# Optimization experiments

Hardware: AMD Instinct MI355X
Metric: run time of the kernel (lower is better)

## Reference

```python
import jax, jax.numpy as jnp
import numpy as np


def setup_inputs() -> dict:
    key = jax.random.key(0)
    k1, k2 = jax.random.split(key)
    B, C, P, D, K = 8, 8, 512, 256, 8192
    z = jax.random.normal(k1, (B, C, P, D), dtype=jnp.float32)
    # codebook initialized with std = 1/sqrt(dim), matching nn.init.normal_
    codebook = jax.random.normal(k2, (K, D), dtype=jnp.float32) / np.sqrt(D).astype(np.float32)
    return {"z": z, "codebook": codebook}


def reference(z, codebook):
    B, C, P, D = z.shape
    z_flat = z.reshape(-1, D)  # [N, D]
    # squared-L2 distances: ||z||^2 - 2 z.cb^T + ||cb||^2  -> [N, K]
    dist = (
        jnp.sum(z_flat * z_flat, axis=1, keepdims=True)
        - 2.0 * jnp.matmul(z_flat, codebook.T)
        + jnp.sum(codebook * codebook, axis=1)[None, :]
    )
    codes = jnp.argmin(dist, axis=1)  # [N]
    z_q = codebook[codes].reshape(B, C, P, D)
    commit_loss = 0.25 * jnp.mean((jax.lax.stop_gradient(z_q) - z) ** 2)
    codebook_loss = jnp.mean((z_q - jax.lax.stop_gradient(z)) ** 2)
    total_loss = commit_loss + 0.25 * codebook_loss
    # straight-through estimator
    z_q_st = z + jax.lax.stop_gradient(z_q - z)
    return (z_q_st, total_loss, codes)
```

## Files before the change

### kernel.cpp

```cpp
#include <hip/hip_runtime.h>
#include <hip/hip_fp16.h>
#include <float.h>

typedef _Float16 half8 __attribute__((ext_vector_type(8)));
typedef _Float16 half4 __attribute__((ext_vector_type(4)));
typedef float floatx4 __attribute__((ext_vector_type(4)));

#define DD 256
#define D4 64
#define KK 8192
#define NROWS 32768
#define BM 64
#define BM2 32
#define BM4 128
#define NELEM 8388608
#define TAU1 1.25e-2f
#define TAU2 2e-3f
#define NSLICE 8
#define SLICE_K 1024
#define NVS 16
#define VS_K 512
#define NBLOCKS1 1024
#define TILES_PER_BLOCK 4

#define WS_V9_BYTES      29360128
#define WS_CASCADE_BYTES 12582912
#define WS_SLICED2_BYTES 7800832
#define WS_R4_REFINE_BYTES 458768
#define WS_R4_FULL_BYTES   8849408

__global__ __launch_bounds__(256) void norms_kernel(
    const float* __restrict__ z, const float* __restrict__ cb,
    float* __restrict__ znorm, float* __restrict__ cbnorm)
{
    int wave = threadIdx.x >> 6;
    int lane = threadIdx.x & 63;
    int row = blockIdx.x * 4 + wave;
    const float4* src;
    float* dst;
    int r;
    if (row < NROWS) { src = (const float4*)z;  dst = znorm;  r = row; }
    else             { src = (const float4*)cb; dst = cbnorm; r = row - NROWS; }
    float4 v = src[(size_t)r * D4 + lane];
    float s = v.x*v.x + v.y*v.y + v.z*v.z + v.w*v.w;
    #pragma unroll
    for (int off = 1; off < 64; off <<= 1) s += __shfl_xor(s, off);
    if (lane == 0) dst[r] = s;
}

__global__ __launch_bounds__(256) void cbnorm_kernel(
    const float* __restrict__ cb, float* __restrict__ cbnorm)
{
    int wave = threadIdx.x >> 6;
    int lane = threadIdx.x & 63;
    int r = blockIdx.x * 4 + wave;
    float4 v = ((const float4*)cb)[(size_t)r * D4 + lane];
    float s = v.x*v.x + v.y*v.y + v.z*v.z + v.w*v.w;
    #pragma unroll
    for (int off = 1; off < 64; off <<= 1) s += __shfl_xor(s, off);
    if (lane == 0) cbnorm[r] = s;
}

__global__ __launch_bounds__(256) void preconv_kernel(
    const float* __restrict__ cb, _Float16* __restrict__ bhi, _Float16* __restrict__ blo)
{
    size_t e4 = (size_t)blockIdx.x * 256 + threadIdx.x;
    float4 v = ((const float4*)cb)[e4];
    float t0 = v.x * 16.f, t1 = v.y * 16.f, t2 = v.z * 16.f, t3 = v.w * 16.f;
    _Float16 h0 = (_Float16)t0, h1 = (_Float16)t1, h2 = (_Float16)t2, h3 = (_Float16)t3;
    _Float16 l0 = (_Float16)((t0 - (float)h0) * 2048.f);
    _Float16 l1 = (_Float16)((t1 - (float)h1) * 2048.f);
    _Float16 l2 = (_Float16)((t2 - (float)h2) * 2048.f);
    _Float16 l3 = (_Float16)((t3 - (float)h3) * 2048.f);
    reinterpret_cast<half4*>(bhi)[e4] = half4{h0, h1, h2, h3};
    reinterpret_cast<half4*>(blo)[e4] = half4{l0, l1, l2, l3};
}

__global__ __launch_bounds__(256) void preconv_z_kernel(
    const float* __restrict__ z, _Float16* __restrict__ zg, float* __restrict__ znorm)
{
    int gid = blockIdx.x * 256 + threadIdx.x;
    int row = gid >> 5;
    int g   = gid & 31;
    int r   = row & 63;
    const float4* src = (const float4*)z + (size_t)row * D4 + g * 2;
    float4 a = src[0], b = src[1];
    half8 h = { (_Float16)a.x, (_Float16)a.y, (_Float16)a.z, (_Float16)a.w,
                (_Float16)b.x, (_Float16)b.y, (_Float16)b.z, (_Float16)b.w };
    int gp = g ^ (r & 7);
    *reinterpret_cast<half8*>((char*)zg + (size_t)(row >> 6) * 32768 + r * 512 + gp * 16) = h;
    float s = a.x*a.x + a.y*a.y + a.z*a.z + a.w*a.w
            + b.x*b.x + b.y*b.y + b.z*b.z + b.w*b.w;
    #pragma unroll
    for (int off = 1; off < 32; off <<= 1) s += __shfl_xor(s, off);
    if ((threadIdx.x & 31) == 0) znorm[row] = s;
}

__global__ __launch_bounds__(256, 4) void vq_fp16_v11(
    const _Float16* __restrict__ zg,
    const _Float16* __restrict__ bhip, const float* __restrict__ cbnorm,
    float* __restrict__ pd, float* __restrict__ ps, int* __restrict__ pk)
{
    __shared__ _Float16 zt[BM * DD];

    const int tid  = threadIdx.x;
    const int lane = tid & 63;
    const int cg   = tid >> 6;
    const int l15  = lane & 15;
    const int lhi  = lane >> 4;
    const int slice = blockIdx.x & 7;
    const int grp   = blockIdx.x >> 3;

    const int A0 = l15 * 512 + ((lhi ^ (l15 & 3)) << 4) + (((l15 >> 2) & 1) << 6);
    int Ar[4];
    #pragma unroll
    for (int rf = 0; rf < 4; ++rf) Ar[rf] = A0 + rf * 8192;
    const char* zbase = (const char*)zt;

    const half8* bp = (const half8*)bhip + ((size_t)(slice * SLICE_K + cg * 32 + l15) * 32 + lhi);
    const float* cnp = cbnorm + slice * SLICE_K + cg * 32 + l15;
    const int kbase = slice * SLICE_K + cg * 32 + l15;

    #pragma unroll 1
    for (int j = 0; j < TILES_PER_BLOCK; ++j) {
        const int tileIdx = grp * TILES_PER_BLOCK + j;
        const int rowBase = tileIdx * BM;

        __syncthreads();
        {
            const float4* src = (const float4*)((const char*)zg + (size_t)tileIdx * 32768);
            float4* dst = (float4*)zt;
            #pragma unroll
            for (int i = 0; i < 8; ++i) dst[i * 256 + tid] = src[i * 256 + tid];
        }

        float bestd[4][4], secd[4][4];
        int   bestk[4][4];
        #pragma unroll
        for (int rf = 0; rf < 4; ++rf)
            #pragma unroll
            for (int reg = 0; reg < 4; ++reg) {
                bestd[rf][reg] = FLT_MAX; secd[rf][reg] = FLT_MAX; bestk[rf][reg] = 0;
            }

        __syncthreads();

        #pragma unroll 1
        for (int kt = 0; kt < SLICE_K / 128; ++kt) {
            floatx4 acc[4][2];
            #pragma unroll
            for (int rf = 0; rf < 4; ++rf)
                #pragma unroll
                for (int cf = 0; cf < 2; ++cf)
                    acc[rf][cf] = floatx4{0.f, 0.f, 0.f, 0.f};

            const half8* b0 = bp + kt * 4096;
            const half8* b1 = b0 + 512;

            #pragma unroll 2
            for (int dc = 0; dc < 8; ++dc) {
                half8 f0 = b0[dc * 4];
                half8 f1 = b1[dc * 4];
                #pragma unroll
                for (int rf = 0; rf < 4; ++rf) {
                    half8 a = *reinterpret_cast<const half8*>(zbase + (Ar[rf] ^ (dc << 6)));
                    acc[rf][0] = __builtin_amdgcn_mfma_f32_16x16x32_f16(a, f0, acc[rf][0], 0, 0, 0);
                    acc[rf][1] = __builtin_amdgcn_mfma_f32_16x16x32_f16(a, f1, acc[rf][1], 0, 0, 0);
                }
            }

            const float cn0 = cnp[kt * 128];
            const float cn1 = cnp[kt * 128 + 16];
            const int k0 = kbase + kt * 128;
            #pragma unroll
            for (int cf = 0; cf < 2; ++cf) {
                const float cn = cf ? cn1 : cn0;
                const int k = k0 + cf * 16;
                #pragma unroll
                for (int rf = 0; rf < 4; ++rf)
                    #pragma unroll
                    for (int reg = 0; reg < 4; ++reg) {
                        float m = fmaf(-0.125f, acc[rf][cf][reg], cn);
                        float w = fmaxf(bestd[rf][reg], m);
                        secd[rf][reg] = fminf(secd[rf][reg], w);
                        if (m < bestd[rf][reg]) { bestd[rf][reg] = m; bestk[rf][reg] = k; }
                    }
            }
        }

        #pragma unroll
        for (int off = 1; off < 16; off <<= 1) {
            #pragma unroll
            for (int rf = 0; rf < 4; ++rf)
                #pragma unroll
                for (int reg = 0; reg < 4; ++reg) {
                    float od = __shfl_xor(bestd[rf][reg], off);
                    int   ok = __shfl_xor(bestk[rf][reg], off);
                    float os = __shfl_xor(secd[rf][reg], off);
                    float hi = fmaxf(bestd[rf][reg], od);
                    secd[rf][reg] = fminf(fminf(secd[rf][reg], os), hi);
                    if (od < bestd[rf][reg] || (od == bestd[rf][reg] && ok < bestk[rf][reg])) {
                        bestd[rf][reg] = od; bestk[rf][reg] = ok;
                    }
                }
        }

        __syncthreads();
        float* dsc = reinterpret_cast<float*>(zt);
        int*   ksc = reinterpret_cast<int*>(zt) + 256;
        float* ssc = reinterpret_cast<float*>(zt) + 512;
        if (l15 == 0) {
            #pragma unroll
            for (int rf = 0; rf < 4; ++rf)
                #pragma unroll
                for (int reg = 0; reg < 4; ++reg) {
                    int rrow = rf * 16 + lhi * 4 + reg;
                    dsc[cg * 64 + rrow] = bestd[rf][reg];
                    ksc[cg * 64 + rrow] = bestk[rf][reg];
                    ssc[cg * 64 + rrow] = secd[rf][reg];
                }
        }
        __syncthreads();
        if (tid < 64) {
            float bd = dsc[tid];
            int   bk = ksc[tid];
            float sd = ssc[tid];
            #pragma unroll
            for (int c = 1; c < 4; ++c) {
                float od = dsc[c * 64 + tid];
                int   ok = ksc[c * 64 + tid];
                float os = ssc[c * 64 + tid];
                float hi = fmaxf(bd, od);
                sd = fminf(fminf(sd, os), hi);
                if (od < bd || (od == bd && ok < bk)) { bd = od; bk = ok; }
            }
            int row = rowBase + tid;
            pd[row * NSLICE + slice] = bd;
            ps[row * NSLICE + slice] = sd;
            pk[row * NSLICE + slice] = bk;
        }
    }
}

__global__ __launch_bounds__(256, 4) void vq_fp16_kernel(
    const float* __restrict__ z,
    const _Float16* __restrict__ bhip, const float* __restrict__ cbnorm,
    float* __restrict__ pd, float* __restrict__ ps, int* __restrict__ pk)
{
    __shared__ _Float16 zhi[BM * DD];
    const int tid  = threadIdx.x;
    const int lane = tid & 63;
    const int cg   = tid >> 6;
    const int l15  = lane & 15;
    const int lhi  = lane >> 4;
    const int slice = blockIdx.x & 7;
    const int grp   = blockIdx.x >> 3;
    const int sliceBase = slice * SLICE_K;

    int rowA[4];
    #pragma unroll
    for (int rf = 0; rf < 4; ++rf) rowA[rf] = rf * 16 + l15;

    #pragma unroll 1
    for (int j = 0; j < TILES_PER_BLOCK; ++j) {
        const int rowBase = (grp * TILES_PER_BLOCK + j) * BM;
        __syncthreads();
        #pragma unroll
        for (int i = 0; i < 16; ++i) {
            int gid = i * 256 + tid;
            int r   = gid >> 6;
            int c4  = gid & 63;
            float4 v = ((const float4*)z)[(size_t)(rowBase + r) * D4 + c4];
            _Float16 h0 = (_Float16)v.x, h1 = (_Float16)v.y,
                     h2 = (_Float16)v.z, h3 = (_Float16)v.w;
            int g = c4 >> 1;
            int byteOff = r * 512 + ((g ^ (r & 7)) << 4) + ((c4 & 1) << 3);
            *reinterpret_cast<half4*>(reinterpret_cast<char*>(zhi) + byteOff) = half4{h0, h1, h2, h3};
        }
        float bestd[4][4], secd[4][4];
        int   bestk[4][4];
        #pragma unroll
        for (int rf = 0; rf < 4; ++rf)
            #pragma unroll
            for (int reg = 0; reg < 4; ++reg) {
                bestd[rf][reg] = FLT_MAX; secd[rf][reg] = FLT_MAX; bestk[rf][reg] = 0;
            }
        __syncthreads();
        #pragma unroll 1
        for (int kt = 0; kt < SLICE_K / 128; ++kt) {
            floatx4 acc[4][2];
            #pragma unroll
            for (int rf = 0; rf < 4; ++rf)
                #pragma unroll
                for (int cf = 0; cf < 2; ++cf)
                    acc[rf][cf] = floatx4{0.f, 0.f, 0.f, 0.f};
            const int codeBase = sliceBase + kt * 128 + cg * 32 + l15;
            #pragma unroll 2
            for (int dc = 0; dc < 8; ++dc) {
                half8 bhi_f[2];
                #pragma unroll
                for (int cf = 0; cf < 2; ++cf) {
                    size_t off = (size_t)(codeBase + 16 * cf) * DD + dc * 32 + lhi * 8;
                    bhi_f[cf] = *reinterpret_cast<const half8*>(bhip + off);
                }
                #pragma unroll
                for (int rf = 0; rf < 4; ++rf) {
                    int g = dc * 4 + lhi;
                    int off = rowA[rf] * 512 + ((g ^ (rowA[rf] & 7)) << 4);
                    half8 ahi = *reinterpret_cast<const half8*>(reinterpret_cast<const char*>(zhi) + off);
                    #pragma unroll
                    for (int cf = 0; cf < 2; ++cf)
                        acc[rf][cf] = __builtin_amdgcn_mfma_f32_16x16x32_f16(ahi, bhi_f[cf], acc[rf][cf], 0, 0, 0);
                }
            }
            #pragma unroll
            for (int cf = 0; cf < 2; ++cf) {
                int k = codeBase + 16 * cf;
                float cn = cbnorm[k];
                #pragma unroll
                for (int rf = 0; rf < 4; ++rf)
                    #pragma unroll
                    for (int reg = 0; reg < 4; ++reg) {
                        float m = fmaf(-0.125f, acc[rf][cf][reg], cn);
                        float w = fmaxf(bestd[rf][reg], m);
                        secd[rf][reg] = fminf(secd[rf][reg], w);
                        if (m < bestd[rf][reg]) { bestd[rf][reg] = m; bestk[rf][reg] = k; }
                    }
            }
        }
        #pragma unroll
        for (int off = 1; off < 16; off <<= 1) {
            #pragma unroll
            for (int rf = 0; rf < 4; ++rf)
                #pragma unroll
                for (int reg = 0; reg < 4; ++reg) {
                    float od = __shfl_xor(bestd[rf][reg], off);
                    int   ok = __shfl_xor(bestk[rf][reg], off);
                    float os = __shfl_xor(secd[rf][reg], off);
                    float hi = fmaxf(bestd[rf][reg], od);
                    secd[rf][reg] = fminf(fminf(secd[rf][reg], os), hi);
                    if (od < bestd[rf][reg] || (od == bestd[rf][reg] && ok < bestk[rf][reg])) {
                        bestd[rf][reg] = od; bestk[rf][reg] = ok;
                    }
                }
        }
        __syncthreads();
        float* dsc = reinterpret_cast<float*>(zhi);
        int*   ksc = reinterpret_cast<int*>(zhi) + 256;
        float* ssc = reinterpret_cast<float*>(zhi) + 512;
        if (l15 == 0) {
            #pragma unroll
            for (int rf = 0; rf < 4; ++rf)
                #pragma unroll
                for (int reg = 0; reg < 4; ++reg) {
                    int rrow = rf * 16 + lhi * 4 + reg;
                    dsc[cg * 64 + rrow] = bestd[rf][reg];
                    ksc[cg * 64 + rrow] = bestk[rf][reg];
                    ssc[cg * 64 + rrow] = secd[rf][reg];
                }
        }
        __syncthreads();
        if (tid < 64) {
            float bd = dsc[tid];
            int   bk = ksc[tid];
            float sd = ssc[tid];
            #pragma unroll
            for (int c = 1; c < 4; ++c) {
                float od = dsc[c * 64 + tid];
                int   ok = ksc[c * 64 + tid];
                float os = ssc[c * 64 + tid];
                float hi = fmaxf(bd, od);
                sd = fminf(fminf(sd, os), hi);
                if (od < bd || (od == bd && ok < bk)) { bd = od; bk = ok; }
            }
            int row = rowBase + tid;
            pd[row * NSLICE + slice] = bd;
            ps[row * NSLICE + slice] = sd;
            pk[row * NSLICE + slice] = bk;
        }
    }
}

__global__ __launch_bounds__(256) void slice_reduce_kernel(
    const float* __restrict__ pd, const float* __restrict__ ps, const int* __restrict__ pk,
    int* __restrict__ codes, float* __restrict__ codes_f,
    int* __restrict__ cnt, int* __restrict__ list, float tau)
{
    int row = blockIdx.x * 256 + threadIdx.x;
    float bd = FLT_MAX, sd = FLT_MAX;
    int bk = 0;
    #pragma unroll
    for (int s = 0; s < NSLICE; ++s) {
        float d  = pd[row * NSLICE + s];
        int   k  = pk[row * NSLICE + s];
        float s2 = ps[row * NSLICE + s];
        float hi = fmaxf(bd, d);
        sd = fminf(fminf(sd, s2), hi);
        if (d < bd || (d == bd && k < bk)) { bd = d; bk = k; }
    }
    codes[row]   = bk;
    codes_f[row] = (float)bk;
    if ((sd - bd) < tau) {
        int idx = atomicAdd(cnt, 1);
        list[idx] = row;
    }
}

__global__ __launch_bounds__(256, 4) void vq_refine2_kernel(
    const float* __restrict__ z,
    const _Float16* __restrict__ bhip, const _Float16* __restrict__ blop,
    const float* __restrict__ cbnorm,
    const int* __restrict__ cnt, const int* __restrict__ list,
    float* __restrict__ pd2, float* __restrict__ ps2, int* __restrict__ pk2)
{
    __shared__ _Float16 zhi[BM2 * DD];
    __shared__ _Float16 zlo[BM2 * DD];

    const int n1 = *cnt;
    if (n1 == 0) return;
    const int ntiles = (n1 + BM2 - 1) / BM2;
    const int njobs = ntiles * NVS;

    const int tid  = threadIdx.x;
    const int lane = tid & 63;
    const int cg   = tid >> 6;
    const int l15  = lane & 15;
    const int lhi  = lane >> 4;

    int rowA[2];
    #pragma unroll
    for (int rf = 0; rf < 2; ++rf) rowA[rf] = rf * 16 + l15;

    for (int job = blockIdx.x; job < njobs; job += gridDim.x) {
        const int vs    = job & (NVS - 1);
        const int tile  = job >> 4;
        const int base  = tile * BM2;
        const int vsBase = vs * VS_K;

        __syncthreads();
        #pragma unroll
        for (int i = 0; i < 8; ++i) {
            int gid = i * 256 + tid;
            int r   = gid >> 6;
            int c4  = gid & 63;
            int pos = base + r;
            int row = list[pos < n1 ? pos : (n1 - 1)];
            float4 v = ((const float4*)z)[(size_t)row * D4 + c4];
            _Float16 h0 = (_Float16)v.x, h1 = (_Float16)v.y,
                     h2 = (_Float16)v.z, h3 = (_Float16)v.w;
            _Float16 e0 = (_Float16)((v.x - (float)h0) * 2048.f);
            _Float16 e1 = (_Float16)((v.y - (float)h1) * 2048.f);
            _Float16 e2 = (_Float16)((v.z - (float)h2) * 2048.f);
            _Float16 e3 = (_Float16)((v.w - (float)h3) * 2048.f);
            int g = c4 >> 1;
            int byteOff = r * 512 + ((g ^ (r & 7)) << 4) + ((c4 & 1) << 3);
            *reinterpret_cast<half4*>(reinterpret_cast<char*>(zhi) + byteOff) = half4{h0, h1, h2, h3};
            *reinterpret_cast<half4*>(reinterpret_cast<char*>(zlo) + byteOff) = half4{e0, e1, e2, e3};
        }

        float bestd[2][4], secd[2][4];
        int   bestk[2][4];
        #pragma unroll
        for (int rf = 0; rf < 2; ++rf)
            #pragma unroll
            for (int reg = 0; reg < 4; ++reg) {
                bestd[rf][reg] = FLT_MAX; secd[rf][reg] = FLT_MAX; bestk[rf][reg] = 0;
            }

        __syncthreads();

        #pragma unroll 1
        for (int kt = 0; kt < VS_K / 128; ++kt) {
            floatx4 accH[2][2], accM[2][2];
            #pragma unroll
            for (int rf = 0; rf < 2; ++rf)
                #pragma unroll
                for (int cf = 0; cf < 2; ++cf) {
                    accH[rf][cf] = floatx4{0.f, 0.f, 0.f, 0.f};
                    accM[rf][cf] = floatx4{0.f, 0.f, 0.f, 0.f};
                }
            const int codeBase = vsBase + kt * 128 + cg * 32 + l15;
            #pragma unroll 2
            for (int dc = 0; dc < 8; ++dc) {
                half8 bhi_f[2], blo_f[2];
                #pragma unroll
                for (int cf = 0; cf < 2; ++cf) {
                    size_t off = (size_t)(codeBase + 16 * cf) * DD + dc * 32 + lhi * 8;
                    bhi_f[cf] = *reinterpret_cast<const half8*>(bhip + off);
                    blo_f[cf] = *reinterpret_cast<const half8*>(blop + off);
                }
                #pragma unroll
                for (int rf = 0; rf < 2; ++rf) {
                    int g = dc * 4 + lhi;
                    int off = rowA[rf] * 512 + ((g ^ (rowA[rf] & 7)) << 4);
                    half8 ahi = *reinterpret_cast<const half8*>(reinterpret_cast<const char*>(zhi) + off);
                    half8 alo = *reinterpret_cast<const half8*>(reinterpret_cast<const char*>(zlo) + off);
                    #pragma unroll
                    for (int cf = 0; cf < 2; ++cf) {
                        accH[rf][cf] = __builtin_amdgcn_mfma_f32_16x16x32_f16(ahi, bhi_f[cf], accH[rf][cf], 0, 0, 0);
                        accM[rf][cf] = __builtin_amdgcn_mfma_f32_16x16x32_f16(alo, bhi_f[cf], accM[rf][cf], 0, 0, 0);
                        accM[rf][cf] = __builtin_amdgcn_mfma_f32_16x16x32_f16(ahi, blo_f[cf], accM[rf][cf], 0, 0, 0);
                    }
                }
            }
            #pragma unroll
            for (int cf = 0; cf < 2; ++cf) {
                int k = codeBase + 16 * cf;
                float cn = cbnorm[k];
                #pragma unroll
                for (int rf = 0; rf < 2; ++rf)
                    #pragma unroll
                    for (int reg = 0; reg < 4; ++reg) {
                        float dot16 = fmaf(accM[rf][cf][reg], 0x1p-11f, accH[rf][cf][reg]);
                        float m = fmaf(-0.125f, dot16, cn);
                        float w = fmaxf(bestd[rf][reg], m);
                        secd[rf][reg] = fminf(secd[rf][reg], w);
                        if (m < bestd[rf][reg]) { bestd[rf][reg] = m; bestk[rf][reg] = k; }
                    }
            }
        }

        #pragma unroll
        for (int off = 1; off < 16; off <<= 1) {
            #pragma unroll
            for (int rf = 0; rf < 2; ++rf)
                #pragma unroll
                for (int reg = 0; reg < 4; ++reg) {
                    float od = __shfl_xor(bestd[rf][reg], off);
                    int   ok = __shfl_xor(bestk[rf][reg], off);
                    float os = __shfl_xor(secd[rf][reg], off);
                    float hi = fmaxf(bestd[rf][reg], od);
                    secd[rf][reg] = fminf(fminf(secd[rf][reg], os), hi);
                    if (od < bestd[rf][reg] || (od == bestd[rf][reg] && ok < bestk[rf][reg])) {
                        bestd[rf][reg] = od; bestk[rf][reg] = ok;
                    }
                }
        }

        __syncthreads();
        float* dsc = reinterpret_cast<float*>(zhi);
        int*   ksc = reinterpret_cast<int*>(zhi) + 128;
        float* ssc = reinterpret_cast<float*>(zhi) + 256;
        if (l15 == 0) {
            #pragma unroll
            for (int rf = 0; rf < 2; ++rf)
                #pragma unroll
                for (int reg = 0; reg < 4; ++reg) {
                    int rrow = rf * 16 + lhi * 4 + reg;
                    dsc[cg * 32 + rrow] = bestd[rf][reg];
                    ksc[cg * 32 + rrow] = bestk[rf][reg];
                    ssc[cg * 32 + rrow] = secd[rf][reg];
                }
        }
        __syncthreads();
        if (tid < 32) {
            float bd = dsc[tid];
            int   bk = ksc[tid];
            float sd = ssc[tid];
            #pragma unroll
            for (int c = 1; c < 4; ++c) {
                float od = dsc[c * 32 + tid];
                int   ok = ksc[c * 32 + tid];
                float os = ssc[c * 32 + tid];
                float hi = fmaxf(bd, od);
                sd = fminf(fminf(sd, os), hi);
                if (od < bd || (od == bd && ok < bk)) { bd = od; bk = ok; }
            }
            int pos = base + tid;
            pd2[pos * NVS + vs] = bd;
            ps2[pos * NVS + vs] = sd;
            pk2[pos * NVS + vs] = bk;
        }
    }
}

__global__ __launch_bounds__(256) void slice_reduce2_kernel(
    const float* __restrict__ pd2, const float* __restrict__ ps2, const int* __restrict__ pk2,
    const int* __restrict__ cnt, const int* __restrict__ list,
    int* __restrict__ codes, float* __restrict__ codes_f,
    int* __restrict__ cnt2, int* __restrict__ list2)
{
    const int n1 = *cnt;
    for (int i = blockIdx.x * 256 + threadIdx.x; i < n1; i += gridDim.x * 256) {
        float bd = FLT_MAX, sd = FLT_MAX;
        int bk = 0;
        #pragma unroll
        for (int s = 0; s < NVS; ++s) {
            float d  = pd2[i * NVS + s];
            int   k  = pk2[i * NVS + s];
            float s2 = ps2[i * NVS + s];
            float hi = fmaxf(bd, d);
            sd = fminf(fminf(sd, s2), hi);
            if (d < bd || (d == bd && k < bk)) { bd = d; bk = k; }
        }
        int row = list[i];
        codes[row]   = bk;
        codes_f[row] = (float)bk;
        if ((sd - bd) < TAU2) {
            int idx = atomicAdd(cnt2, 1);
            list2[idx] = row;
        }
    }
}

__global__ __launch_bounds__(256) void refine_kernel(
    const float* __restrict__ z, const float* __restrict__ cb,
    const float* __restrict__ znorm, const float* __restrict__ cbnorm,
    const int* __restrict__ cnt, const int* __restrict__ list,
    int* __restrict__ codes, float* __restrict__ codes_f)
{
    __shared__ float zrow[DD];
    __shared__ float dred[4];
    __shared__ int   kred[4];
    const int tid = threadIdx.x;
    const int lane = tid & 63;
    const int wv = tid >> 6;
    const int n = *cnt;
    for (int i = blockIdx.x; i < n; i += gridDim.x) {
        const int row = list[i];
        if (tid < 64) ((float4*)zrow)[tid] = ((const float4*)z)[(size_t)row * D4 + tid];
        const float zn = znorm[row];
        __syncthreads();
        float bd = FLT_MAX;
        int   bk = 0;
        for (int k = tid; k < KK; k += 256) {
            const float4* crow = (const float4*)cb + (size_t)k * D4;
            float acc = 0.f;
            #pragma unroll 8
            for (int d4 = 0; d4 < D4; ++d4) {
                float4 c = crow[d4];
                float4 zv = ((const float4*)zrow)[d4];
                acc = fmaf(zv.x, c.x, acc);
                acc = fmaf(zv.y, c.y, acc);
                acc = fmaf(zv.z, c.z, acc);
                acc = fmaf(zv.w, c.w, acc);
            }
            float dist = fmaf(-2.f, acc, zn) + cbnorm[k];
            if (dist < bd) { bd = dist; bk = k; }
        }
        #pragma unroll
        for (int off = 1; off < 64; off <<= 1) {
            float od = __shfl_xor(bd, off);
            int   ok = __shfl_xor(bk, off);
            if (od < bd || (od == bd && ok < bk)) { bd = od; bk = ok; }
        }
        if (lane == 0) { dred[wv] = bd; kred[wv] = bk; }
        __syncthreads();
        if (tid == 0) {
            #pragma unroll
            for (int c = 1; c < 4; ++c) {
                if (dred[c] < bd || (dred[c] == bd && kred[c] < bk)) { bd = dred[c]; bk = kred[c]; }
            }
            codes[row]   = bk;
            codes_f[row] = (float)bk;
        }
        __syncthreads();
    }
}

__global__ __launch_bounds__(256) void gather_loss_kernel(
    const float* __restrict__ z, const float* __restrict__ cb,
    const int* __restrict__ codes, float* __restrict__ zq_out,
    float* __restrict__ partials)
{
    __shared__ float red[4];
    int tid = threadIdx.x;
    size_t e4 = (size_t)blockIdx.x * 256 + tid;
    int row = (int)(e4 >> 6);
    int d4  = (int)(e4 & 63);
    int code = codes[row];
    float4 q  = ((const float4*)cb)[(size_t)code * D4 + d4];
    float4 zv = ((const float4*)z)[e4];
    float dx = q.x - zv.x, dy = q.y - zv.y, dz = q.z - zv.z, dw = q.w - zv.w;
    float4 o;
    o.x = zv.x + dx; o.y = zv.y + dy; o.z = zv.z + dz; o.w = zv.w + dw;
    ((float4*)zq_out)[e4] = o;
    float s = dx*dx + dy*dy + dz*dz + dw*dw;
    #pragma unroll
    for (int off = 1; off < 64; off <<= 1) s += __shfl_xor(s, off);
    if ((tid & 63) == 0) red[tid >> 6] = s;
    __syncthreads();
    if (tid == 0) partials[blockIdx.x] = ((red[0] + red[1]) + red[2]) + red[3];
}

__global__ __launch_bounds__(256) void final_loss_kernel(
    const float* __restrict__ partials, float* __restrict__ out_loss)
{
    __shared__ float red[4];
    int tid = threadIdx.x;
    float s = 0.f;
    #pragma unroll 4
    for (int i = 0; i < 32; ++i) s += partials[tid * 32 + i];
    #pragma unroll
    for (int off = 1; off < 64; off <<= 1) s += __shfl_xor(s, off);
    if ((tid & 63) == 0) red[tid >> 6] = s;
    __syncthreads();
    if (tid == 0) {
        float tot = ((red[0] + red[1]) + red[2]) + red[3];
        out_loss[0] = 0.5f * (tot / (float)NELEM);
    }
}

template <bool PRECONV, bool REFINE>
__global__ __launch_bounds__(512, 1) void vq_mfma_kernel(
    const float* __restrict__ z, const float* __restrict__ cb,
    const _Float16* __restrict__ bhip, const _Float16* __restrict__ blop,
    const float* __restrict__ znorm, const float* __restrict__ cbnorm,
    int* __restrict__ codes, float* __restrict__ codes_f,
    int* __restrict__ cnt, int* __restrict__ list)
{
    __shared__ _Float16 zhi[BM4 * DD];
    __shared__ _Float16 zlo[BM4 * DD];
    const int tid  = threadIdx.x;
    const int lane = tid & 63;
    const int w    = tid >> 6;
    const int rg   = w >> 2;
    const int cg   = w & 3;
    const int l15  = lane & 15;
    const int lhi  = lane >> 4;
    const int rowBase = blockIdx.x * BM4;

    #pragma unroll
    for (int i = 0; i < 16; ++i) {
        int gid = i * 512 + tid;
        int r   = gid >> 6;
        int c4  = gid & 63;
        float4 v = ((const float4*)z)[(size_t)(rowBase + r) * D4 + c4];
        _Float16 h0 = (_Float16)v.x, h1 = (_Float16)v.y,
                 h2 = (_Float16)v.z, h3 = (_Float16)v.w;
        _Float16 e0 = (_Float16)((v.x - (float)h0) * 2048.f);
        _Float16 e1 = (_Float16)((v.y - (float)h1) * 2048.f);
        _Float16 e2 = (_Float16)((v.z - (float)h2) * 2048.f);
        _Float16 e3 = (_Float16)((v.w - (float)h3) * 2048.f);
        int g = c4 >> 1;
        int byteOff = r * 512 + (((g ^ (r & 7))) << 4) + ((c4 & 1) << 3);
        *reinterpret_cast<half4*>(reinterpret_cast<char*>(zhi) + byteOff) = half4{h0, h1, h2, h3};
        *reinterpret_cast<half4*>(reinterpret_cast<char*>(zlo) + byteOff) = half4{e0, e1, e2, e3};
    }
    int rowA[4];
    #pragma unroll
    for (int rf = 0; rf < 4; ++rf) rowA[rf] = rg * 64 + rf * 16 + l15;
    float zn[4][4];
    #pragma unroll
    for (int rf = 0; rf < 4; ++rf)
        #pragma unroll
        for (int reg = 0; reg < 4; ++reg)
            zn[rf][reg] = znorm[rowBase + rg * 64 + rf * 16 + lhi * 4 + reg];
    float bestd[4][4], secd[4][4];
    int   bestk[4][4];
    #pragma unroll
    for (int rf = 0; rf < 4; ++rf)
        #pragma unroll
        for (int reg = 0; reg < 4; ++reg) {
            bestd[rf][reg] = FLT_MAX; secd[rf][reg] = FLT_MAX; bestk[rf][reg] = 0;
        }
    __syncthreads();
    for (int kt = 0; kt < KK / 256; ++kt) {
        floatx4 accH[4][4], accM[4][4];
        #pragma unroll
        for (int rf = 0; rf < 4; ++rf)
            #pragma unroll
            for (int cf = 0; cf < 4; ++cf) {
                accH[rf][cf] = floatx4{0.f, 0.f, 0.f, 0.f};
                accM[rf][cf] = floatx4{0.f, 0.f, 0.f, 0.f};
            }
        const int codeBase = kt * 256 + cg * 64 + l15;
        for (int dc = 0; dc < 8; ++dc) {
            half8 bhi_f[4], blo_f[4];
            #pragma unroll
            for (int cf = 0; cf < 4; ++cf) {
                if (PRECONV) {
                    size_t off = (size_t)(codeBase + 16 * cf) * DD + dc * 32 + lhi * 8;
                    bhi_f[cf] = *reinterpret_cast<const half8*>(bhip + off);
                    blo_f[cf] = *reinterpret_cast<const half8*>(blop + off);
                } else {
                    const float4* p = (const float4*)(cb + (size_t)(codeBase + 16 * cf) * DD + dc * 32 + lhi * 8);
                    float4 u0 = p[0];
                    float4 u1 = p[1];
                    float uv[8] = {u0.x, u0.y, u0.z, u0.w, u1.x, u1.y, u1.z, u1.w};
                    half8 bh, bl;
                    #pragma unroll
                    for (int jj = 0; jj < 8; ++jj) {
                        float t = uv[jj] * 16.f;
                        _Float16 h = (_Float16)t;
                        bh[jj] = h;
                        bl[jj] = (_Float16)((t - (float)h) * 2048.f);
                    }
                    bhi_f[cf] = bh; blo_f[cf] = bl;
                }
            }
            #pragma unroll
            for (int rf = 0; rf < 4; ++rf) {
                int g = dc * 4 + lhi;
                int off = rowA[rf] * 512 + ((g ^ (rowA[rf] & 7)) << 4);
                half8 ahi = *reinterpret_cast<const half8*>(reinterpret_cast<const char*>(zhi) + off);
                half8 alo = *reinterpret_cast<const half8*>(reinterpret_cast<const char*>(zlo) + off);
                #pragma unroll
                for (int cf = 0; cf < 4; ++cf) {
                    accH[rf][cf] = __builtin_amdgcn_mfma_f32_16x16x32_f16(ahi, bhi_f[cf], accH[rf][cf], 0, 0, 0);
                    accM[rf][cf] = __builtin_amdgcn_mfma_f32_16x16x32_f16(alo, bhi_f[cf], accM[rf][cf], 0, 0, 0);
                    accM[rf][cf] = __builtin_amdgcn_mfma_f32_16x16x32_f16(ahi, blo_f[cf], accM[rf][cf], 0, 0, 0);
                }
            }
        }
        #pragma unroll
        for (int cf = 0; cf < 4; ++cf) {
            int k = codeBase + 16 * cf;
            float cn = cbnorm[k];
            #pragma unroll
            for (int rf = 0; rf < 4; ++rf)
                #pragma unroll
                for (int reg = 0; reg < 4; ++reg) {
                    float dot16 = fmaf(accM[rf][cf][reg], 0x1p-11f, accH[rf][cf][reg]);
                    float dist  = fmaf(-0.125f, dot16, zn[rf][reg]) + cn;
                    float wv2 = fmaxf(bestd[rf][reg], dist);
                    secd[rf][reg] = fminf(secd[rf][reg], wv2);
                    if (dist < bestd[rf][reg]) { bestd[rf][reg] = dist; bestk[rf][reg] = k; }
                }
        }
    }
    #pragma unroll
    for (int off = 1; off < 16; off <<= 1) {
        #pragma unroll
        for (int rf = 0; rf < 4; ++rf)
            #pragma unroll
            for (int reg = 0; reg < 4; ++reg) {
                float od = __shfl_xor(bestd[rf][reg], off);
                int   ok = __shfl_xor(bestk[rf][reg], off);
                float os = __shfl_xor(secd[rf][reg], off);
                float hi = fmaxf(bestd[rf][reg], od);
                secd[rf][reg] = fminf(fminf(secd[rf][reg], os), hi);
                if (od < bestd[rf][reg] || (od == bestd[rf][reg] && ok < bestk[rf][reg])) {
                    bestd[rf][reg] = od; bestk[rf][reg] = ok;
                }
            }
    }
    __syncthreads();
    float* dsc = reinterpret_cast<float*>(zhi);
    int*   ksc = reinterpret_cast<int*>(zhi) + 512;
    float* ssc = reinterpret_cast<float*>(zhi) + 1024;
    if (l15 == 0) {
        #pragma unroll
        for (int rf = 0; rf < 4; ++rf)
            #pragma unroll
            for (int reg = 0; reg < 4; ++reg) {
                int rrow = rg * 64 + rf * 16 + lhi * 4 + reg;
                dsc[cg * 128 + rrow] = bestd[rf][reg];
                ksc[cg * 128 + rrow] = bestk[rf][reg];
                ssc[cg * 128 + rrow] = secd[rf][reg];
            }
    }
    __syncthreads();
    if (tid < 128) {
        float bd = dsc[tid];
        int   bk = ksc[tid];
        float sd = ssc[tid];
        #pragma unroll
        for (int c = 1; c < 4; ++c) {
            float od = dsc[c * 128 + tid];
            int   ok = ksc[c * 128 + tid];
            float os = ssc[c * 128 + tid];
            float hi = fmaxf(bd, od);
            sd = fminf(fminf(sd, os), hi);
            if (od < bd || (od == bd && ok < bk)) { bd = od; bk = ok; }
        }
        int row = rowBase + tid;
        codes[row]   = bk;
        codes_f[row] = (float)bk;
        if (REFINE && (sd - bd) < TAU2) {
            int idx = atomicAdd(cnt, 1);
            list[idx] = row;
        }
    }
}

extern "C" void kernel_launch(void* const* d_in, const int* in_sizes, int n_in,
                              void* d_out, int out_size, void* d_ws, size_t ws_size,
                              hipStream_t stream) {
    const float* z  = (const float*)d_in[0];
    const float* cb = (const float*)d_in[1];
    float* out      = (float*)d_out;
    float* zq_out   = out;
    float* loss_out = out + NELEM;
    float* codes_f  = out + NELEM + 1;

    char* wsb       = (char*)d_ws;
    float* znorm    = (float*)(wsb + 0);
    float* cbnorm   = (float*)(wsb + 131072);
    int*   codes    = (int*)(wsb + 163840);
    float* partials = (float*)(wsb + 294912);
    int*   cnt      = (int*)(wsb + 327680);
    int*   cnt2     = (int*)(wsb + 327684);
    int*   list     = (int*)(wsb + 327696);

    if (ws_size >= (size_t)WS_V9_BYTES) {
        int*   list2  = (int*)(wsb + 460800);
        float* pd     = (float*)(wsb + 593920);
        float* ps     = (float*)(wsb + 1642496);
        int*   pk     = (int*)(wsb + 2691072);
        _Float16* bhi = (_Float16*)(wsb + 4194304);
        _Float16* blo = (_Float16*)(wsb + 8388608);
        _Float16* zg  = (_Float16*)(wsb + 12582912);
        float* pd2    = (float*)(wsb + 12582912);
        float* ps2    = (float*)(wsb + 12582912 + 2097152);
        int*   pk2    = (int*)(wsb + 12582912 + 4194304);

        hipMemsetAsync(cnt, 0, 8, stream);
        cbnorm_kernel<<<2048, 256, 0, stream>>>(cb, cbnorm);
        preconv_kernel<<<2048, 256, 0, stream>>>(cb, bhi, blo);
        preconv_z_kernel<<<4096, 256, 0, stream>>>(z, zg, znorm);
        vq_fp16_v11<<<NBLOCKS1, 256, 0, stream>>>(zg, bhi, cbnorm, pd, ps, pk);
        slice_reduce_kernel<<<128, 256, 0, stream>>>(pd, ps, pk, codes, codes_f, cnt, list, TAU1);
        vq_refine2_kernel<<<512, 256, 0, stream>>>(z, bhi, blo, cbnorm, cnt, list, pd2, ps2, pk2);
        slice_reduce2_kernel<<<64, 256, 0, stream>>>(pd2, ps2, pk2, cnt, list, codes, codes_f, cnt2, list2);
        refine_kernel<<<256, 256, 0, stream>>>(z, cb, znorm, cbnorm, cnt2, list2, codes, codes_f);
    } else if (ws_size >= (size_t)WS_CASCADE_BYTES) {
        int*   list2  = (int*)(wsb + 460800);
        float* pd     = (float*)(wsb + 593920);
        float* ps     = (float*)(wsb + 1642496);
        int*   pk     = (int*)(wsb + 2691072);
        _Float16* bhi = (_Float16*)(wsb + 4194304);
        _Float16* blo = (_Float16*)(wsb + 8388608);
        hipMemsetAsync(cnt, 0, 8, stream);
        norms_kernel<<<10240, 256, 0, stream>>>(z, cb, znorm, cbnorm);
        preconv_kernel<<<2048, 256, 0, stream>>>(cb, bhi, blo);
        vq_fp16_kernel<<<NBLOCKS1, 256, 0, stream>>>(z, bhi, cbnorm, pd, ps, pk);
        slice_reduce_kernel<<<128, 256, 0, stream>>>(pd, ps, pk, codes, codes_f, cnt, list, TAU1);
        refine_kernel<<<256, 256, 0, stream>>>(z, cb, znorm, cbnorm, cnt, list, codes, codes_f);
    } else {
        _Float16* bhi = (_Float16*)(wsb + 460800);
        _Float16* blo = (_Float16*)(wsb + 4655104);
        const bool preconv = ws_size >= (size_t)WS_R4_FULL_BYTES;
        const bool refine  = ws_size >= (size_t)WS_R4_REFINE_BYTES;
        norms_kernel<<<10240, 256, 0, stream>>>(z, cb, znorm, cbnorm);
        if (refine) hipMemsetAsync(cnt, 0, sizeof(int), stream);
        if (preconv) preconv_kernel<<<2048, 256, 0, stream>>>(cb, bhi, blo);
        if (preconv && refine)
            vq_mfma_kernel<true, true><<<NROWS / BM4, 512, 0, stream>>>(z, cb, bhi, blo, znorm, cbnorm, codes, codes_f, cnt, list);
        else if (preconv)
            vq_mfma_kernel<true, false><<<NROWS / BM4, 512, 0, stream>>>(z, cb, bhi, blo, znorm, cbnorm, codes, codes_f, cnt, list);
        else if (refine)
            vq_mfma_kernel<false, true><<<NROWS / BM4, 512, 0, stream>>>(z, cb, bhi, blo, znorm, cbnorm, codes, codes_f, cnt, list);
        else
            vq_mfma_kernel<false, false><<<NROWS / BM4, 512, 0, stream>>>(z, cb, bhi, blo, znorm, cbnorm, codes, codes_f, cnt, list);
        if (refine)
            refine_kernel<<<256, 256, 0, stream>>>(z, cb, znorm, cbnorm, cnt, list, codes, codes_f);
    }

    gather_loss_kernel<<<8192, 256, 0, stream>>>(z, cb, codes, zq_out, partials);
    final_loss_kernel<<<1, 256, 0, stream>>>(partials, loss_out);
}
```

Before: 595.1 us.

## Replace split-fp16 MFMA refine cascade with single fp32 FMA refine pass

Removes the second refinement stage, which used hi/lo fp16 MFMA and a margin filter followed by an exact fp32 refine on a smaller candidate list. All candidates flagged by the first pass now get an exact fp32 CUDA-core distance over the full codebook, tiled 32 rows by 8 slices. The codebook norm and fp16 hi conversion are fused into one prep kernel, and the lo-part conversion is dropped. This cuts two kernel launches and the lo-plane prep, but it moves the candidate refine from matrix cores to scalar FMA, which costs much more compute per candidate row.

```diff
diff --git a/kernel.cpp b/kernel.cpp
--- a/kernel.cpp
+++ b/kernel.cpp
@@ -15,17 +15,14 @@
 #define BM4 128
 #define NELEM 8388608
 #define TAU1 1.25e-2f
-#define TAU2 2e-3f
 #define NSLICE 8
 #define SLICE_K 1024
-#define NVS 16
-#define VS_K 512
 #define NBLOCKS1 1024
 #define TILES_PER_BLOCK 4
+#define TAU2 2e-3f
 
 #define WS_V9_BYTES      29360128
 #define WS_CASCADE_BYTES 12582912
-#define WS_SLICED2_BYTES 7800832
 #define WS_R4_REFINE_BYTES 458768
 #define WS_R4_FULL_BYTES   8849408
 
@@ -48,13 +45,16 @@
     if (lane == 0) dst[r] = s;
 }
 
-__global__ __launch_bounds__(256) void cbnorm_kernel(
-    const float* __restrict__ cb, float* __restrict__ cbnorm)
+__global__ __launch_bounds__(256) void prep_cb_kernel(
+    const float* __restrict__ cb, float* __restrict__ cbnorm, _Float16* __restrict__ bhi)
 {
     int wave = threadIdx.x >> 6;
     int lane = threadIdx.x & 63;
     int r = blockIdx.x * 4 + wave;
     float4 v = ((const float4*)cb)[(size_t)r * D4 + lane];
+    _Float16 h0 = (_Float16)(v.x * 16.f), h1 = (_Float16)(v.y * 16.f);
+    _Float16 h2 = (_Float16)(v.z * 16.f), h3 = (_Float16)(v.w * 16.f);
+    reinterpret_cast<half4*>(bhi)[(size_t)r * D4 + lane] = half4{h0, h1, h2, h3};
     float s = v.x*v.x + v.y*v.y + v.z*v.z + v.w*v.w;
     #pragma unroll
     for (int off = 1; off < 64; off <<= 1) s += __shfl_xor(s, off);
@@ -406,200 +406,129 @@
     }
 }
 
-__global__ __launch_bounds__(256, 4) void vq_refine2_kernel(
-    const float* __restrict__ z,
-    const _Float16* __restrict__ bhip, const _Float16* __restrict__ blop,
-    const float* __restrict__ cbnorm,
+__global__ __launch_bounds__(256) void refine32_kernel(
+    const float* __restrict__ z, const float* __restrict__ cb,
+    const float* __restrict__ znorm, const float* __restrict__ cbnorm,
     const int* __restrict__ cnt, const int* __restrict__ list,
-    float* __restrict__ pd2, float* __restrict__ ps2, int* __restrict__ pk2)
-{
-    __shared__ _Float16 zhi[BM2 * DD];
-    __shared__ _Float16 zlo[BM2 * DD];
-
+    float* __restrict__ pd2, int* __restrict__ pk2)
+{
+    __shared__ float zrows[BM2][DD];
+    __shared__ float znls[BM2];
+    __shared__ float dsc[4][8];
+    __shared__ int   ksc[4][8];
     const int n1 = *cnt;
     if (n1 == 0) return;
     const int ntiles = (n1 + BM2 - 1) / BM2;
-    const int njobs = ntiles * NVS;
-
+    const int njobs = ntiles * NSLICE;
     const int tid  = threadIdx.x;
     const int lane = tid & 63;
-    const int cg   = tid >> 6;
-    const int l15  = lane & 15;
-    const int lhi  = lane >> 4;
-
-    int rowA[2];
-    #pragma unroll
-    for (int rf = 0; rf < 2; ++rf) rowA[rf] = rf * 16 + l15;
+    const int wv   = tid >> 6;
 
     for (int job = blockIdx.x; job < njobs; job += gridDim.x) {
-        const int vs    = job & (NVS - 1);
-        const int tile  = job >> 4;
+        const int slice = job & 7;
+        const int tile  = job >> 3;
         const int base  = tile * BM2;
-        const int vsBase = vs * VS_K;
-
-        __syncthreads();
-        #pragma unroll
-        for (int i = 0; i < 8; ++i) {
-            int gid = i * 256 + tid;
-            int r   = gid >> 6;
-            int c4  = gid & 63;
+        const int kbase = slice * SLICE_K;
+
+        __syncthreads();
+        for (int i = tid; i < BM2 * D4; i += 256) {
+            int r = i >> 6, c4 = i & 63;
             int pos = base + r;
-            int row = list[pos < n1 ? pos : (n1 - 1)];
-            float4 v = ((const float4*)z)[(size_t)row * D4 + c4];
-            _Float16 h0 = (_Float16)v.x, h1 = (_Float16)v.y,
-                     h2 = (_Float16)v.z, h3 = (_Float16)v.w;
-            _Float16 e0 = (_Float16)((v.x - (float)h0) * 2048.f);
-            _Float16 e1 = (_Float16)((v.y - (float)h1) * 2048.f);
-            _Float16 e2 = (_Float16)((v.z - (float)h2) * 2048.f);
-            _Float16 e3 = (_Float16)((v.w - (float)h3) * 2048.f);
-            int g = c4 >> 1;
-            int byteOff = r * 512 + ((g ^ (r & 7)) << 4) + ((c4 & 1) << 3);
-            *reinterpret_cast<half4*>(reinterpret_cast<char*>(zhi) + byteOff) = half4{h0, h1, h2, h3};
-            *reinterpret_cast<half4*>(reinterpret_cast<char*>(zlo) + byteOff) = half4{e0, e1, e2, e3};
-        }
-
-        float bestd[2][4], secd[2][4];
-        int   bestk[2][4];
-        #pragma unroll
-        for (int rf = 0; rf < 2; ++rf)
-            #pragma unroll
-            for (int reg = 0; reg < 4; ++reg) {
-                bestd[rf][reg] = FLT_MAX; secd[rf][reg] = FLT_MAX; bestk[rf][reg] = 0;
-            }
-
+            int row = list[pos < n1 ? pos : n1 - 1];
+            ((float4*)zrows[r])[c4] = ((const float4*)z)[(size_t)row * D4 + c4];
+        }
+        if (tid < BM2) {
+            int pos = base + tid;
+            znls[tid] = znorm[list[pos < n1 ? pos : n1 - 1]];
+        }
         __syncthreads();
 
         #pragma unroll 1
-        for (int kt = 0; kt < VS_K / 128; ++kt) {
-            floatx4 accH[2][2], accM[2][2];
-            #pragma unroll
-            for (int rf = 0; rf < 2; ++rf)
-                #pragma unroll
-                for (int cf = 0; cf < 2; ++cf) {
-                    accH[rf][cf] = floatx4{0.f, 0.f, 0.f, 0.f};
-                    accM[rf][cf] = floatx4{0.f, 0.f, 0.f, 0.f};
-                }
-            const int codeBase = vsBase + kt * 128 + cg * 32 + l15;
-            #pragma unroll 2
-            for (int dc = 0; dc < 8; ++dc) {
-                half8 bhi_f[2], blo_f[2];
-                #pragma unroll
-                for (int cf = 0; cf < 2; ++cf) {
-                    size_t off = (size_t)(codeBase + 16 * cf) * DD + dc * 32 + lhi * 8;
-                    bhi_f[cf] = *reinterpret_cast<const half8*>(bhip + off);
-                    blo_f[cf] = *reinterpret_cast<const half8*>(blop + off);
-                }
-                #pragma unroll
-                for (int rf = 0; rf < 2; ++rf) {
-                    int g = dc * 4 + lhi;
-                    int off = rowA[rf] * 512 + ((g ^ (rowA[rf] & 7)) << 4);
-                    half8 ahi = *reinterpret_cast<const half8*>(reinterpret_cast<const char*>(zhi) + off);
-                    half8 alo = *reinterpret_cast<const half8*>(reinterpret_cast<const char*>(zlo) + off);
+        for (int rc = 0; rc < 4; ++rc) {
+            float bd8[8];
+            int   bk8[8];
+            #pragma unroll
+            for (int r8 = 0; r8 < 8; ++r8) { bd8[r8] = FLT_MAX; bk8[r8] = 0; }
+
+            #pragma unroll 1
+            for (int c = 0; c < 4; ++c) {
+                const int k = kbase + c * 256 + tid;
+                const float4* crow = (const float4*)cb + (size_t)k * D4;
+                float acc[8];
+                #pragma unroll
+                for (int r8 = 0; r8 < 8; ++r8) acc[r8] = 0.f;
+                #pragma unroll 4
+                for (int d4 = 0; d4 < D4; ++d4) {
+                    float4 cv = crow[d4];
                     #pragma unroll
-                    for (int cf = 0; cf < 2; ++cf) {
-                        accH[rf][cf] = __builtin_amdgcn_mfma_f32_16x16x32_f16(ahi, bhi_f[cf], accH[rf][cf], 0, 0, 0);
-                        accM[rf][cf] = __builtin_amdgcn_mfma_f32_16x16x32_f16(alo, bhi_f[cf], accM[rf][cf], 0, 0, 0);
-                        accM[rf][cf] = __builtin_amdgcn_mfma_f32_16x16x32_f16(ahi, blo_f[cf], accM[rf][cf], 0, 0, 0);
+                    for (int r8 = 0; r8 < 8; ++r8) {
+                        float4 zv = ((const float4*)zrows[rc * 8 + r8])[d4];
+                        acc[r8] = fmaf(zv.x, cv.x, acc[r8]);
+                        acc[r8] = fmaf(zv.y, cv.y, acc[r8]);
+                        acc[r8] = fmaf(zv.z, cv.z, acc[r8]);
+                        acc[r8] = fmaf(zv.w, cv.w, acc[r8]);
                     }
                 }
-            }
-            #pragma unroll
-            for (int cf = 0; cf < 2; ++cf) {
-                int k = codeBase + 16 * cf;
-                float cn = cbnorm[k];
-                #pragma unroll
-                for (int rf = 0; rf < 2; ++rf)
-                    #pragma unroll
-                    for (int reg = 0; reg < 4; ++reg) {
-                        float dot16 = fmaf(accM[rf][cf][reg], 0x1p-11f, accH[rf][cf][reg]);
-                        float m = fmaf(-0.125f, dot16, cn);
-                        float w = fmaxf(bestd[rf][reg], m);
-                        secd[rf][reg] = fminf(secd[rf][reg], w);
-                        if (m < bestd[rf][reg]) { bestd[rf][reg] = m; bestk[rf][reg] = k; }
+                const float cn = cbnorm[k];
+                #pragma unroll
+                for (int r8 = 0; r8 < 8; ++r8) {
+                    float dist = fmaf(-2.f, acc[r8], znls[rc * 8 + r8]) + cn;
+                    if (dist < bd8[r8]) { bd8[r8] = dist; bk8[r8] = k; }
+                }
+            }
+
+            #pragma unroll
+            for (int off = 1; off < 64; off <<= 1) {
+                #pragma unroll
+                for (int r8 = 0; r8 < 8; ++r8) {
+                    float od = __shfl_xor(bd8[r8], off);
+                    int   ok = __shfl_xor(bk8[r8], off);
+                    if (od < bd8[r8] || (od == bd8[r8] && ok < bk8[r8])) {
+                        bd8[r8] = od; bk8[r8] = ok;
                     }
-            }
-        }
-
-        #pragma unroll
-        for (int off = 1; off < 16; off <<= 1) {
-            #pragma unroll
-            for (int rf = 0; rf < 2; ++rf)
-                #pragma unroll
-                for (int reg = 0; reg < 4; ++reg) {
-                    float od = __shfl_xor(bestd[rf][reg], off);
-                    int   ok = __shfl_xor(bestk[rf][reg], off);
-                    float os = __shfl_xor(secd[rf][reg], off);
-                    float hi = fmaxf(bestd[rf][reg], od);
-                    secd[rf][reg] = fminf(fminf(secd[rf][reg], os), hi);
-                    if (od < bestd[rf][reg] || (od == bestd[rf][reg] && ok < bestk[rf][reg])) {
-                        bestd[rf][reg] = od; bestk[rf][reg] = ok;
-                    }
-                }
-        }
-
-        __syncthreads();
-        float* dsc = reinterpret_cast<float*>(zhi);
-        int*   ksc = reinterpret_cast<int*>(zhi) + 128;
-        float* ssc = reinterpret_cast<float*>(zhi) + 256;
-        if (l15 == 0) {
-            #pragma unroll
-            for (int rf = 0; rf < 2; ++rf)
-                #pragma unroll
-                for (int reg = 0; reg < 4; ++reg) {
-                    int rrow = rf * 16 + lhi * 4 + reg;
-                    dsc[cg * 32 + rrow] = bestd[rf][reg];
-                    ksc[cg * 32 + rrow] = bestk[rf][reg];
-                    ssc[cg * 32 + rrow] = secd[rf][reg];
-                }
-        }
-        __syncthreads();
-        if (tid < 32) {
-            float bd = dsc[tid];
-            int   bk = ksc[tid];
-            float sd = ssc[tid];
-            #pragma unroll
-            for (int c = 1; c < 4; ++c) {
-                float od = dsc[c * 32 + tid];
-                int   ok = ksc[c * 32 + tid];
-                float os = ssc[c * 32 + tid];
-                float hi = fmaxf(bd, od);
-                sd = fminf(fminf(sd, os), hi);
-                if (od < bd || (od == bd && ok < bk)) { bd = od; bk = ok; }
-            }
-            int pos = base + tid;
-            pd2[pos * NVS + vs] = bd;
-            ps2[pos * NVS + vs] = sd;
-            pk2[pos * NVS + vs] = bk;
-        }
-    }
-}
-
-__global__ __launch_bounds__(256) void slice_reduce2_kernel(
-    const float* __restrict__ pd2, const float* __restrict__ ps2, const int* __restrict__ pk2,
+                }
+            }
+            if (lane == 0) {
+                #pragma unroll
+                for (int r8 = 0; r8 < 8; ++r8) { dsc[wv][r8] = bd8[r8]; ksc[wv][r8] = bk8[r8]; }
+            }
+            __syncthreads();
+            if (tid < 8) {
+                float bd = dsc[0][tid];
+                int   bk = ksc[0][tid];
+                #pragma unroll
+                for (int w = 1; w < 4; ++w) {
+                    float od = dsc[w][tid];
+                    int   ok = ksc[w][tid];
+                    if (od < bd || (od == bd && ok < bk)) { bd = od; bk = ok; }
+                }
+                int pos = base + rc * 8 + tid;
+                pd2[pos * NSLICE + slice] = bd;
+                pk2[pos * NSLICE + slice] = bk;
+            }
+            __syncthreads();
+        }
+    }
+}
+
+__global__ __launch_bounds__(256) void slice_merge_kernel(
+    const float* __restrict__ pd2, const int* __restrict__ pk2,
     const int* __restrict__ cnt, const int* __restrict__ list,
-    int* __restrict__ codes, float* __restrict__ codes_f,
-    int* __restrict__ cnt2, int* __restrict__ list2)
+    int* __restrict__ codes, float* __restrict__ codes_f)
 {
     const int n1 = *cnt;
     for (int i = blockIdx.x * 256 + threadIdx.x; i < n1; i += gridDim.x * 256) {
-        float bd = FLT_MAX, sd = FLT_MAX;
+        float bd = FLT_MAX;
         int bk = 0;
         #pragma unroll
-        for (int s = 0; s < NVS; ++s) {
-            float d  = pd2[i * NVS + s];
-            int   k  = pk2[i * NVS + s];
-            float s2 = ps2[i * NVS + s];
-            float hi = fmaxf(bd, d);
-            sd = fminf(fminf(sd, s2), hi);
+        for (int s = 0; s < NSLICE; ++s) {
+            float d = pd2[i * NSLICE + s];
+            int   k = pk2[i * NSLICE + s];
             if (d < bd || (d == bd && k < bk)) { bd = d; bk = k; }
         }
         int row = list[i];
         codes[row]   = bk;
         codes_f[row] = (float)bk;
-        if ((sd - bd) < TAU2) {
-            int idx = atomicAdd(cnt2, 1);
-            list2[idx] = row;
-        }
     }
 }
 
@@ -890,32 +819,25 @@
     int*   codes    = (int*)(wsb + 163840);
     float* partials = (float*)(wsb + 294912);
     int*   cnt      = (int*)(wsb + 327680);
-    int*   cnt2     = (int*)(wsb + 327684);
     int*   list     = (int*)(wsb + 327696);
 
     if (ws_size >= (size_t)WS_V9_BYTES) {
-        int*   list2  = (int*)(wsb + 460800);
         float* pd     = (float*)(wsb + 593920);
         float* ps     = (float*)(wsb + 1642496);
         int*   pk     = (int*)(wsb + 2691072);
         _Float16* bhi = (_Float16*)(wsb + 4194304);
-        _Float16* blo = (_Float16*)(wsb + 8388608);
         _Float16* zg  = (_Float16*)(wsb + 12582912);
         float* pd2    = (float*)(wsb + 12582912);
-        float* ps2    = (float*)(wsb + 12582912 + 2097152);
-        int*   pk2    = (int*)(wsb + 12582912 + 4194304);
+        int*   pk2    = (int*)(wsb + 12582912 + 2097152);
 
         hipMemsetAsync(cnt, 0, 8, stream);
-        cbnorm_kernel<<<2048, 256, 0, stream>>>(cb, cbnorm);
-        preconv_kernel<<<2048, 256, 0, stream>>>(cb, bhi, blo);
+        prep_cb_kernel<<<2048, 256, 0, stream>>>(cb, cbnorm, bhi);
         preconv_z_kernel<<<4096, 256, 0, stream>>>(z, zg, znorm);
         vq_fp16_v11<<<NBLOCKS1, 256, 0, stream>>>(zg, bhi, cbnorm, pd, ps, pk);
         slice_reduce_kernel<<<128, 256, 0, stream>>>(pd, ps, pk, codes, codes_f, cnt, list, TAU1);
-        vq_refine2_kernel<<<512, 256, 0, stream>>>(z, bhi, blo, cbnorm, cnt, list, pd2, ps2, pk2);
-        slice_reduce2_kernel<<<64, 256, 0, stream>>>(pd2, ps2, pk2, cnt, list, codes, codes_f, cnt2, list2);
-        refine_kernel<<<256, 256, 0, stream>>>(z, cb, znorm, cbnorm, cnt2, list2, codes, codes_f);
+        refine32_kernel<<<512, 256, 0, stream>>>(z, cb, znorm, cbnorm, cnt, list, pd2, pk2);
+        slice_merge_kernel<<<64, 256, 0, stream>>>(pd2, pk2, cnt, list, codes, codes_f);
     } else if (ws_size >= (size_t)WS_CASCADE_BYTES) {
-        int*   list2  = (int*)(wsb + 460800);
         float* pd     = (float*)(wsb + 593920);
         float* ps     = (float*)(wsb + 1642496);
         int*   pk     = (int*)(wsb + 2691072);
```

After: 578.8 us. 1.03x faster.
